# Performance work log

Hardware: AMD Instinct MI355X
Metric: run time of the kernel (lower is better)

Reference implementation:

```python
import jax, jax.numpy as jnp
import numpy as np

B = 262144
D = 16          # input_dim
D2 = D // 2     # 8, == hidden_dim
H = 8           # hidden_dim
L = 15          # num_layers (couplings)
NH = 3          # hidden_block_layers
EPS = 1e-6
SLOPE = 0.01    # LeakyReLU default


def setup_inputs() -> dict:
    key = jax.random.key(0)
    ks = jax.random.split(key, 8)
    z = jax.random.normal(ks[0], (B, D), dtype=jnp.float32)
    s = 0.2  # keep log_s away from the +/-5 clamp saturation
    W_in = jax.random.normal(ks[1], (L, 2, D2, H), dtype=jnp.float32) * s
    b_in = jax.random.normal(ks[2], (L, 2, H), dtype=jnp.float32) * s
    W_hid = jax.random.normal(ks[3], (L, 2, NH, H, H), dtype=jnp.float32) * s
    b_hid = jax.random.normal(ks[4], (L, 2, NH, H), dtype=jnp.float32) * s
    W_out = jax.random.normal(ks[5], (L, 2, H, D2), dtype=jnp.float32) * s
    b_out = jax.random.normal(ks[6], (L, 2, D2), dtype=jnp.float32) * s
    # 14 random permutations between couplings + identity after the last coupling
    rng = np.random.default_rng(0)
    perms = np.stack([rng.permutation(D) for _ in range(L - 1)] + [np.arange(D)])
    perms = jnp.asarray(perms, dtype=jnp.int32)  # [L, D]
    return {"z": z, "W_in": W_in, "b_in": b_in, "W_hid": W_hid,
            "b_hid": b_hid, "W_out": W_out, "b_out": b_out, "perms": perms}


def _mlp(x, Wi, bi, Wh, bh, Wo, bo):
    # LinearBlock: (Linear+LeakyReLU) + NH x (Linear+LeakyReLU) + Linear
    h = jax.nn.leaky_relu(x @ Wi + bi, SLOPE)
    for j in range(NH):  # NH is a small static constant
        h = jax.nn.leaky_relu(h @ Wh[j] + bh[j], SLOPE)
    return h @ Wo + bo


def _flow(z, W_in, b_in, W_hid, b_hid, W_out, b_out, perms):
    def step(carry, params):
        z, ld = carry
        Wi, bi, Wh, bh, Wo, bo, perm = params
        z_l, z_r = z[:, :D2], z[:, D2:]
        log_s = jnp.clip(_mlp(z_l, Wi[0], bi[0], Wh[0], bh[0], Wo[0], bo[0]), -5.0, 5.0)
        b = _mlp(z_l, Wi[1], bi[1], Wh[1], bh[1], Wo[1], bo[1])
        y_r = (jnp.exp(log_s) + EPS) * z_r + b
        y = jnp.concatenate([z_l, y_r], axis=1)
        ld = ld + jnp.sum(log_s, axis=1)
        y = y[:, perm]  # Permutation layer (identity for the last step)
        return (y, ld), None

    ld0 = jnp.zeros(z.shape[0], dtype=z.dtype)
    (y, ld), _ = jax.lax.scan(step, (z, ld0), (W_in, b_in, W_hid, b_hid, W_out, b_out, perms))
    return y, ld


def reference(z, W_in, b_in, W_hid, b_hid, W_out, b_out, perms):
    return _flow(z, W_in, b_in, W_hid, b_hid, W_out, b_out, perms)
```

## Files before the change

### kernel.cpp

```cpp
#include <hip/hip_runtime.h>

#define BN 262144
#define S4 4
#define QS (BN / S4)
#define LNUM 15
#define NSTG 151
#define NF4 (NSTG * 18)

extern "C" __global__ void build_slab(
    const float* __restrict__ Wi, const float* __restrict__ bi,
    const float* __restrict__ Wh, const float* __restrict__ bh,
    const float* __restrict__ Wo, const float* __restrict__ bo,
    float* __restrict__ slab) {
    int idx = blockIdx.x * 256 + threadIdx.x;
    if (idx >= NSTG * 72) return;
    int sl = idx / 72, k = idx % 72;
    if (sl == NSTG - 1) sl = 0;
    const int l = sl / 10, r = sl % 10, net = r / 5, st = r % 5;
    const int nb = l * 2 + net;
    float v;
    if (k < 8) {
        if (st == 0)      v = bi[nb * 8 + k];
        else if (st < 4)  v = bh[(nb * 3 + (st - 1)) * 8 + k];
        else              v = bo[nb * 8 + k];
    } else {
        const int kk = k - 8;
        if (st == 0)      v = Wi[nb * 64 + kk];
        else if (st < 4)  v = Wh[(nb * 3 + (st - 1)) * 64 + kk];
        else              v = Wo[nb * 64 + kk];
    }
    slab[idx] = v;
}

#define GB(gb, k) ((k) % 4 == 0 ? gb[(k) / 4].x : (k) % 4 == 1 ? gb[(k) / 4].y \
                 : (k) % 4 == 2 ? gb[(k) / 4].z : gb[(k) / 4].w)

#define CHA(IN, OUT)                                                          \
    {                                                                         \
        _Pragma("unroll") for (int o = 0; o < 8; ++o) {                       \
            const float bb = GB(B0, o);                                       \
            const float w0 = GB(B0, 8 + o), w1 = GB(B0, 16 + o);              \
            _Pragma("unroll") for (int s = 0; s < 4; ++s)                     \
                OUT[s][o] = fmaf(IN[s][1], w1, fmaf(IN[s][0], w0, bb));       \
        }                                                                     \
        _Pragma("unroll") for (int j = 0; j < 6; ++j) B0[j] = gptr[j];        \
        gptr += 6;                                                            \
        __builtin_amdgcn_sched_barrier(0);                                    \
    }
#define CHB(IN, OUT)                                                          \
    {                                                                         \
        _Pragma("unroll") for (int o = 0; o < 8; ++o) {                       \
            const float w2 = GB(B1, o), w3 = GB(B1, 8 + o), w4 = GB(B1, 16 + o); \
            _Pragma("unroll") for (int s = 0; s < 4; ++s)                     \
                OUT[s][o] = fmaf(IN[s][4], w4,                                 \
                             fmaf(IN[s][3], w3, fmaf(IN[s][2], w2, OUT[s][o]))); \
        }                                                                     \
        _Pragma("unroll") for (int j = 0; j < 6; ++j) B1[j] = gptr[j];        \
        gptr += 6;                                                            \
        __builtin_amdgcn_sched_barrier(0);                                    \
    }
#define CHC(IN, OUT, DOLR)                                                    \
    {                                                                         \
        _Pragma("unroll") for (int o = 0; o < 8; ++o) {                       \
            const float w5 = GB(B2, o), w6 = GB(B2, 8 + o), w7 = GB(B2, 16 + o); \
            _Pragma("unroll") for (int s = 0; s < 4; ++s) {                   \
                float a = fmaf(IN[s][7], w7,                                   \
                            fmaf(IN[s][6], w6, fmaf(IN[s][5], w5, OUT[s][o]))); \
                OUT[s][o] = (DOLR) ? fmaxf(a, 0.01f * a) : a;                 \
            }                                                                 \
        }                                                                     \
        _Pragma("unroll") for (int j = 0; j < 6; ++j) B2[j] = gptr[j];        \
        gptr += 6;                                                            \
        __builtin_amdgcn_sched_barrier(0);                                    \
    }
#define STG(IN, OUT, DOLR) CHA(IN, OUT) CHB(IN, OUT) CHC(IN, OUT, DOLR)

extern "C" __global__ void __launch_bounds__(256, 1) flow_fwd(
    const float* __restrict__ z, const float* __restrict__ slab,
    const int* __restrict__ perms,
    float* __restrict__ outy, float* __restrict__ outld) {
    __shared__ float4 wls[NF4];
    __shared__ float xs[256 * 69];
    __shared__ int pls[LNUM * 16];
    const int t = threadIdx.x;
    const int i0 = blockIdx.x * 256 + t;

    {
        const float4* gs = reinterpret_cast<const float4*>(slab);
        for (int k = t; k < NF4; k += 256) wls[k] = gs[k];
        if (t < LNUM * 16) pls[t] = perms[t];
    }

    float x[4][16];
#pragma unroll
    for (int s = 0; s < 4; ++s) {
        const float4* zp = reinterpret_cast<const float4*>(z + (long)(i0 + s * QS) * 16);
#pragma unroll
        for (int q = 0; q < 4; ++q) {
            float4 a = zp[q];
            x[s][4 * q] = a.x; x[s][4 * q + 1] = a.y;
            x[s][4 * q + 2] = a.z; x[s][4 * q + 3] = a.w;
        }
    }
    float ld[4] = {0.f, 0.f, 0.f, 0.f};
    __syncthreads();

    float4 B0[6], B1[6], B2[6];
    const float4* gptr = wls;
#pragma unroll
    for (int j = 0; j < 6; ++j) B0[j] = gptr[j];
    gptr += 6;
#pragma unroll
    for (int j = 0; j < 6; ++j) B1[j] = gptr[j];
    gptr += 6;
#pragma unroll
    for (int j = 0; j < 6; ++j) B2[j] = gptr[j];
    gptr += 6;
    __builtin_amdgcn_sched_barrier(0);

#pragma unroll 1
    for (int l = 0; l < LNUM; ++l) {
        float h[4][8], g[4][8], sf[4][8], bf[4][8];
        STG(x, h, 1) STG(h, g, 1) STG(g, h, 1) STG(h, g, 1) STG(g, sf, 0)
        STG(x, h, 1) STG(h, g, 1) STG(g, h, 1) STG(h, g, 1) STG(g, bf, 0)

#pragma unroll
        for (int s = 0; s < 4; ++s)
#pragma unroll
            for (int k = 0; k < 8; ++k) {
                const float cs = fminf(fmaxf(sf[s][k], -5.f), 5.f);
                ld[s] += cs;
                x[s][8 + k] = fmaf(__expf(cs) + 1e-6f, x[s][8 + k], bf[s][k]);
            }
        float* __restrict__ ms = &xs[t * 69];
#pragma unroll
        for (int s = 0; s < 4; ++s)
#pragma unroll
            for (int p = 0; p < 16; ++p) ms[s * 17 + p] = x[s][p];
        const int* __restrict__ pl = pls + l * 16;
#pragma unroll
        for (int j = 0; j < 16; ++j) {
            const int pj = pl[j];
#pragma unroll
            for (int s = 0; s < 4; ++s) x[s][j] = ms[s * 17 + pj];
        }
    }

#pragma unroll
    for (int s = 0; s < 4; ++s) {
        float4* ya = reinterpret_cast<float4*>(outy + (long)(i0 + s * QS) * 16);
#pragma unroll
        for (int q = 0; q < 4; ++q) {
            float4 a;
            a.x = x[s][4 * q]; a.y = x[s][4 * q + 1];
            a.z = x[s][4 * q + 2]; a.w = x[s][4 * q + 3];
            ya[q] = a;
        }
        outld[i0 + s * QS] = ld[s];
    }
}

extern "C" void kernel_launch(void* const* d_in, const int* in_sizes, int n_in,
                              void* d_out, int out_size, void* d_ws, size_t ws_size,
                              hipStream_t stream) {
    const float* z = (const float*)d_in[0];
    const float* Wi = (const float*)d_in[1];
    const float* bi = (const float*)d_in[2];
    const float* Wh = (const float*)d_in[3];
    const float* bh = (const float*)d_in[4];
    const float* Wo = (const float*)d_in[5];
    const float* bo = (const float*)d_in[6];
    const int* perms = (const int*)d_in[7];
    float* out = (float*)d_out;
    float* slab = (float*)d_ws;

    hipLaunchKernelGGL(build_slab, dim3((NSTG * 72 + 255) / 256), dim3(256), 0, stream,
                       Wi, bi, Wh, bh, Wo, bo, slab);
    hipLaunchKernelGGL(flow_fwd, dim3(QS / 256), dim3(256), 0, stream,
                       z, slab, perms, out, out + (size_t)BN * 16);
}
```

Before: 119.6 us.

## Keep rows in LDS with composed permutations, halve rows per thread, use exp2

Each thread's row state now stays in shared memory, and a small kernel composes the permutations once so each coupling reads and writes through index offsets instead of permuting a register copy. The per-thread batch drops from 4 rows to 2 and blocks grow to 512 threads, trading instruction-level parallelism for occupancy. The log-scale output layer is prescaled by log2(e) so the kernel can call the hardware exp2 and rescale the log-det by ln2 at the end. An extra launch and LDS read/write traffic per element are added, and the prescaling may change floating-point rounding slightly.

```diff
diff --git a/kernel.cpp b/kernel.cpp
--- a/kernel.cpp
+++ b/kernel.cpp
@@ -1,11 +1,13 @@
 #include <hip/hip_runtime.h>
 
 #define BN 262144
-#define S4 4
-#define QS (BN / S4)
+#define HALF (BN / 2)
 #define LNUM 15
 #define NSTG 151
 #define NF4 (NSTG * 18)
+#define LOG2E 1.4426950408889634f
+#define LN2 0.6931471805599453f
+#define L2CLIP 7.2134752044448170f
 
 extern "C" __global__ void build_slab(
     const float* __restrict__ Wi, const float* __restrict__ bi,
@@ -18,145 +20,149 @@
     if (sl == NSTG - 1) sl = 0;
     const int l = sl / 10, r = sl % 10, net = r / 5, st = r % 5;
     const int nb = l * 2 + net;
+    const float sc = (net == 0 && st == 4) ? LOG2E : 1.0f;
     float v;
     if (k < 8) {
         if (st == 0)      v = bi[nb * 8 + k];
         else if (st < 4)  v = bh[(nb * 3 + (st - 1)) * 8 + k];
-        else              v = bo[nb * 8 + k];
+        else              v = bo[nb * 8 + k] * sc;
     } else {
         const int kk = k - 8;
         if (st == 0)      v = Wi[nb * 64 + kk];
         else if (st < 4)  v = Wh[(nb * 3 + (st - 1)) * 64 + kk];
-        else              v = Wo[nb * 64 + kk];
+        else              v = Wo[nb * 64 + kk] * sc;
     }
     slab[idx] = v;
+}
+
+extern "C" __global__ void compose_perms(const int* __restrict__ perms, int* __restrict__ c) {
+    if (threadIdx.x != 0 || blockIdx.x != 0) return;
+    int cur[16];
+    for (int j = 0; j < 16; ++j) { cur[j] = j; c[j] = j; }
+    for (int l = 0; l < LNUM; ++l) {
+        int nx[16];
+        for (int j = 0; j < 16; ++j) nx[j] = cur[perms[l * 16 + j]];
+        for (int j = 0; j < 16; ++j) { c[(l + 1) * 16 + j] = nx[j]; cur[j] = nx[j]; }
+    }
 }
 
 #define GB(gb, k) ((k) % 4 == 0 ? gb[(k) / 4].x : (k) % 4 == 1 ? gb[(k) / 4].y \
                  : (k) % 4 == 2 ? gb[(k) / 4].z : gb[(k) / 4].w)
 
-#define CHA(IN, OUT)                                                          \
+#define CHA(IN, OUT, BUF)                                                     \
     {                                                                         \
         _Pragma("unroll") for (int o = 0; o < 8; ++o) {                       \
-            const float bb = GB(B0, o);                                       \
-            const float w0 = GB(B0, 8 + o), w1 = GB(B0, 16 + o);              \
-            _Pragma("unroll") for (int s = 0; s < 4; ++s)                     \
+            const float bb = GB(BUF, o);                                      \
+            const float w0 = GB(BUF, 8 + o), w1 = GB(BUF, 16 + o);            \
+            _Pragma("unroll") for (int s = 0; s < 2; ++s)                     \
                 OUT[s][o] = fmaf(IN[s][1], w1, fmaf(IN[s][0], w0, bb));       \
         }                                                                     \
-        _Pragma("unroll") for (int j = 0; j < 6; ++j) B0[j] = gptr[j];        \
+        _Pragma("unroll") for (int j = 0; j < 6; ++j) BUF[j] = gptr[j];       \
         gptr += 6;                                                            \
         __builtin_amdgcn_sched_barrier(0);                                    \
     }
-#define CHB(IN, OUT)                                                          \
+#define CHB(IN, OUT, BUF)                                                     \
     {                                                                         \
         _Pragma("unroll") for (int o = 0; o < 8; ++o) {                       \
-            const float w2 = GB(B1, o), w3 = GB(B1, 8 + o), w4 = GB(B1, 16 + o); \
-            _Pragma("unroll") for (int s = 0; s < 4; ++s)                     \
+            const float w2 = GB(BUF, o), w3 = GB(BUF, 8 + o), w4 = GB(BUF, 16 + o); \
+            _Pragma("unroll") for (int s = 0; s < 2; ++s)                     \
                 OUT[s][o] = fmaf(IN[s][4], w4,                                 \
                              fmaf(IN[s][3], w3, fmaf(IN[s][2], w2, OUT[s][o]))); \
         }                                                                     \
-        _Pragma("unroll") for (int j = 0; j < 6; ++j) B1[j] = gptr[j];        \
+        _Pragma("unroll") for (int j = 0; j < 6; ++j) BUF[j] = gptr[j];       \
         gptr += 6;                                                            \
         __builtin_amdgcn_sched_barrier(0);                                    \
     }
-#define CHC(IN, OUT, DOLR)                                                    \
+#define CHC(IN, OUT, BUF, DOLR)                                               \
     {                                                                         \
         _Pragma("unroll") for (int o = 0; o < 8; ++o) {                       \
-            const float w5 = GB(B2, o), w6 = GB(B2, 8 + o), w7 = GB(B2, 16 + o); \
-            _Pragma("unroll") for (int s = 0; s < 4; ++s) {                   \
+            const float w5 = GB(BUF, o), w6 = GB(BUF, 8 + o), w7 = GB(BUF, 16 + o); \
+            _Pragma("unroll") for (int s = 0; s < 2; ++s) {                   \
                 float a = fmaf(IN[s][7], w7,                                   \
                             fmaf(IN[s][6], w6, fmaf(IN[s][5], w5, OUT[s][o]))); \
                 OUT[s][o] = (DOLR) ? fmaxf(a, 0.01f * a) : a;                 \
             }                                                                 \
         }                                                                     \
-        _Pragma("unroll") for (int j = 0; j < 6; ++j) B2[j] = gptr[j];        \
+        _Pragma("unroll") for (int j = 0; j < 6; ++j) BUF[j] = gptr[j];       \
         gptr += 6;                                                            \
         __builtin_amdgcn_sched_barrier(0);                                    \
     }
-#define STG(IN, OUT, DOLR) CHA(IN, OUT) CHB(IN, OUT) CHC(IN, OUT, DOLR)
+#define STG(IN, OUT, DOLR) CHA(IN, OUT, B0) CHB(IN, OUT, B1) CHC(IN, OUT, B2, DOLR)
 
-extern "C" __global__ void __launch_bounds__(256, 1) flow_fwd(
+extern "C" __global__ void __launch_bounds__(512) flow_fwd(
     const float* __restrict__ z, const float* __restrict__ slab,
-    const int* __restrict__ perms,
+    const int* __restrict__ cperm,
     float* __restrict__ outy, float* __restrict__ outld) {
     __shared__ float4 wls[NF4];
-    __shared__ float xs[256 * 69];
-    __shared__ int pls[LNUM * 16];
+    __shared__ float xs[512 * 33];
     const int t = threadIdx.x;
-    const int i0 = blockIdx.x * 256 + t;
+    const long i = (long)blockIdx.x * 512 + t;
+    float* __restrict__ myx = &xs[t * 33];
 
     {
         const float4* gs = reinterpret_cast<const float4*>(slab);
-        for (int k = t; k < NF4; k += 256) wls[k] = gs[k];
-        if (t < LNUM * 16) pls[t] = perms[t];
+        for (int k = t; k < NF4; k += 512) wls[k] = gs[k];
     }
-
-    float x[4][16];
-#pragma unroll
-    for (int s = 0; s < 4; ++s) {
-        const float4* zp = reinterpret_cast<const float4*>(z + (long)(i0 + s * QS) * 16);
+    {
+        const float4* zp = reinterpret_cast<const float4*>(z + i * 16);
+        const float4* zq = reinterpret_cast<const float4*>(z + (i + HALF) * 16);
 #pragma unroll
         for (int q = 0; q < 4; ++q) {
-            float4 a = zp[q];
-            x[s][4 * q] = a.x; x[s][4 * q + 1] = a.y;
-            x[s][4 * q + 2] = a.z; x[s][4 * q + 3] = a.w;
+            float4 a = zp[q], b = zq[q];
+            myx[4 * q] = a.x; myx[4 * q + 1] = a.y; myx[4 * q + 2] = a.z; myx[4 * q + 3] = a.w;
+            myx[16 + 4 * q] = b.x; myx[17 + 4 * q] = b.y; myx[18 + 4 * q] = b.z; myx[19 + 4 * q] = b.w;
         }
     }
-    float ld[4] = {0.f, 0.f, 0.f, 0.f};
+    float ld2A = 0.f, ld2B = 0.f;
     __syncthreads();
 
     float4 B0[6], B1[6], B2[6];
-    const float4* gptr = wls;
 #pragma unroll
-    for (int j = 0; j < 6; ++j) B0[j] = gptr[j];
-    gptr += 6;
-#pragma unroll
-    for (int j = 0; j < 6; ++j) B1[j] = gptr[j];
-    gptr += 6;
-#pragma unroll
-    for (int j = 0; j < 6; ++j) B2[j] = gptr[j];
-    gptr += 6;
+    for (int j = 0; j < 6; ++j) { B0[j] = wls[j]; B1[j] = wls[6 + j]; B2[j] = wls[12 + j]; }
+    const float4* gptr = wls + 18;
     __builtin_amdgcn_sched_barrier(0);
 
 #pragma unroll 1
     for (int l = 0; l < LNUM; ++l) {
-        float h[4][8], g[4][8], sf[4][8], bf[4][8];
-        STG(x, h, 1) STG(h, g, 1) STG(g, h, 1) STG(h, g, 1) STG(g, sf, 0)
-        STG(x, h, 1) STG(h, g, 1) STG(g, h, 1) STG(h, g, 1) STG(g, bf, 0)
+        const int* __restrict__ cl = cperm + l * 16;
+        float in2[2][8];
+#pragma unroll
+        for (int j = 0; j < 8; ++j) {
+            const int off = cl[j];
+            in2[0][j] = myx[off];
+            in2[1][j] = myx[16 + off];
+        }
+        float h[2][8], g[2][8], sf[2][8], bf[2][8];
+        STG(in2, h, 1) STG(h, g, 1) STG(g, h, 1) STG(h, g, 1) STG(g, sf, 0)
+        STG(in2, h, 1) STG(h, g, 1) STG(g, h, 1) STG(h, g, 1) STG(g, bf, 0)
 
 #pragma unroll
-        for (int s = 0; s < 4; ++s)
-#pragma unroll
-            for (int k = 0; k < 8; ++k) {
-                const float cs = fminf(fmaxf(sf[s][k], -5.f), 5.f);
-                ld[s] += cs;
-                x[s][8 + k] = fmaf(__expf(cs) + 1e-6f, x[s][8 + k], bf[s][k]);
-            }
-        float* __restrict__ ms = &xs[t * 69];
-#pragma unroll
-        for (int s = 0; s < 4; ++s)
-#pragma unroll
-            for (int p = 0; p < 16; ++p) ms[s * 17 + p] = x[s][p];
-        const int* __restrict__ pl = pls + l * 16;
-#pragma unroll
-        for (int j = 0; j < 16; ++j) {
-            const int pj = pl[j];
-#pragma unroll
-            for (int s = 0; s < 4; ++s) x[s][j] = ms[s * 17 + pj];
+        for (int k = 0; k < 8; ++k) {
+            const int off = cl[8 + k];
+            const float cA = fminf(fmaxf(sf[0][k], -L2CLIP), L2CLIP);
+            const float cB = fminf(fmaxf(sf[1][k], -L2CLIP), L2CLIP);
+            ld2A += cA; ld2B += cB;
+            myx[off]      = fmaf(__builtin_amdgcn_exp2f(cA) + 1e-6f, myx[off],      bf[0][k]);
+            myx[16 + off] = fmaf(__builtin_amdgcn_exp2f(cB) + 1e-6f, myx[16 + off], bf[1][k]);
         }
     }
 
-#pragma unroll
-    for (int s = 0; s < 4; ++s) {
-        float4* ya = reinterpret_cast<float4*>(outy + (long)(i0 + s * QS) * 16);
+    {
+        const int* __restrict__ cf = cperm + LNUM * 16;
+        float4 oa[4], ob[4];
 #pragma unroll
         for (int q = 0; q < 4; ++q) {
-            float4 a;
-            a.x = x[s][4 * q]; a.y = x[s][4 * q + 1];
-            a.z = x[s][4 * q + 2]; a.w = x[s][4 * q + 3];
-            ya[q] = a;
+            const int c0 = cf[4 * q], c1 = cf[4 * q + 1], c2 = cf[4 * q + 2], c3 = cf[4 * q + 3];
+            oa[q].x = myx[c0]; oa[q].y = myx[c1]; oa[q].z = myx[c2]; oa[q].w = myx[c3];
+            ob[q].x = myx[16 + c0]; ob[q].y = myx[16 + c1];
+            ob[q].z = myx[16 + c2]; ob[q].w = myx[16 + c3];
         }
-        outld[i0 + s * QS] = ld[s];
+        float4* ya = reinterpret_cast<float4*>(outy + i * 16);
+        float4* yb = reinterpret_cast<float4*>(outy + (i + HALF) * 16);
+#pragma unroll
+        for (int q = 0; q < 4; ++q) { ya[q] = oa[q]; yb[q] = ob[q]; }
+        outld[i] = ld2A * LN2;
+        outld[i + HALF] = ld2B * LN2;
     }
 }
 
@@ -173,9 +179,11 @@
     const int* perms = (const int*)d_in[7];
     float* out = (float*)d_out;
     float* slab = (float*)d_ws;
+    int* cperm = (int*)(slab + NSTG * 72);
 
     hipLaunchKernelGGL(build_slab, dim3((NSTG * 72 + 255) / 256), dim3(256), 0, stream,
                        Wi, bi, Wh, bh, Wo, bo, slab);
-    hipLaunchKernelGGL(flow_fwd, dim3(QS / 256), dim3(256), 0, stream,
-                       z, slab, perms, out, out + (size_t)BN * 16);
+    hipLaunchKernelGGL(compose_perms, dim3(1), dim3(64), 0, stream, perms, cperm);
+    hipLaunchKernelGGL(flow_fwd, dim3(HALF / 512), dim3(512), 0, stream,
+                       z, slab, cperm, out, out + (size_t)BN * 16);
 }
```

Result: faster. 95.93 us (median of 2 runs) (-19.8%).
